# Performance work log

Measured on AMD Instinct MI355X. Metric: run time of the kernel, lower is better.

The kernel has to match this reference:

```python
import jax, jax.numpy as jnp
import numpy as np

N = 64        # n_nodes per graph
H = 128       # hidden channels (128x0e + 128x1o)
NB = 8        # radial bessel basis size
L = 2         # num_interactions
R_MAX = 5.0
AVG_NEIGH = 63.0
DIM = 3       # output vector dim
B = 64        # batch (vmapped)
T = 32        # time-embedding dim
S = 5         # num_species


def _edges(n):
    # fully-connected graph, no self loops (static shapes, jit-friendly)
    s, r = np.meshgrid(np.arange(n), np.arange(n), indexing='ij')
    m = s != r
    return jnp.asarray(s[m]), jnp.asarray(r[m])


def setup_inputs() -> dict:
    key = jax.random.key(0)
    ks = jax.random.split(key, 12)
    sc = 0.05
    return {
        'positions': jax.random.normal(ks[0], (B, N, 3), jnp.float32),
        'node_features': jax.random.randint(ks[1], (B, N), 0, S).astype(jnp.int64),
        'global_features': jax.random.normal(ks[2], (B, T), jnp.float32),
        'emb': jax.random.normal(ks[3], (S, H), jnp.float32) * sc,
        'Wt': jax.random.normal(ks[4], (T, H), jnp.float32) * sc,
        'Wr1': jax.random.normal(ks[5], (L, NB, H), jnp.float32) * sc,
        'Wr2': jax.random.normal(ks[6], (L, H, H), jnp.float32) * sc,
        'Wupd': jax.random.normal(ks[7], (L, H, H), jnp.float32) * sc,
        'Wmix': jax.random.normal(ks[8], (L, H, H), jnp.float32) * sc,
        'Wg1': jax.random.normal(ks[9], (H, H), jnp.float32) * sc,
        'Wg2': jax.random.normal(ks[10], (H, H), jnp.float32) * sc,
        'final_scaling': jnp.ones((), jnp.float32),
    }


def _call_single(pos, z, t, emb, Wt, Wr1, Wr2, Wupd, Wmix, Wg1, Wg2, final_scaling):
    snd, rcv = _edges(N)
    ev = pos[rcv] - pos[snd]                               # [E,3] edge vectors (gather)
    r = jnp.sqrt(jnp.sum(ev * ev, axis=-1) + 1e-12)        # [E]
    u = ev / r[:, None]                                    # unit directions
    # Bessel radial basis with cosine cutoff (r_max acts as soft radius graph)
    n = jnp.arange(1, NB + 1, dtype=pos.dtype)
    rb = jnp.sin(n * jnp.pi * r[:, None] / R_MAX) / r[:, None]   # [E,NB]
    fc = 0.5 * (jnp.cos(jnp.pi * r / R_MAX) + 1.0) * (r < R_MAX)
    rb = rb * fc[:, None]
    # node embedding from species + time embedding
    h = emb[z] + t @ Wt                                    # [N,H] scalar features
    v = jnp.zeros((N, H, DIM), pos.dtype)                  # vector (1o) features
    for l in range(L):
        w = jax.nn.silu(rb @ Wr1[l]) @ Wr2[l]              # [E,H] radial weights
        m0 = w * h[snd]                                    # [E,H] scalar messages
        m1 = m0[:, :, None] * u[:, None, :]                # [E,H,3] vector messages
        a0 = jax.ops.segment_sum(m0, rcv, num_segments=N) / AVG_NEIGH
        a1 = jax.ops.segment_sum(m1, rcv, num_segments=N) / AVG_NEIGH
        h = h + a0 @ Wupd[l]
        v = v + jnp.einsum('ngd,gh->nhd', a1, Wmix[l])
    # equivariant readout: scalar gate per channel contracts vector channels
    g = jax.nn.silu(h @ Wg1) @ Wg2                         # [N,H]
    out = jnp.einsum('nhd,nh->nd', v, g)                   # [N,3]
    return out * final_scaling


def reference(positions, node_features, global_features, emb, Wt, Wr1, Wr2, Wupd, Wmix, Wg1, Wg2, final_scaling):
    f = lambda p, z, t: _call_single(p, z, t, emb, Wt, Wr1, Wr2, Wupd, Wmix, Wg1, Wg2, final_scaling)
    return jax.vmap(f)(positions, node_features, global_features)
```

## Files before the change

kernel.cpp:

```cpp
#include <hip/hip_runtime.h>
#include <math.h>

#define NN 64
#define HH 128
#define NBB 8
#define TT 32
#define BB 64
#define NROW (BB * NN)
#define PLANE ((size_t)NROW * HH)
#define WR1OFF (8 * 16384)

typedef __attribute__((ext_vector_type(8))) short short8;
typedef __attribute__((ext_vector_type(4))) short s16x4;
typedef __attribute__((ext_vector_type(4))) float f32x4;
typedef __attribute__((ext_vector_type(2))) float f32x2;
typedef __attribute__((ext_vector_type(2))) unsigned int u32x2;

__device__ __forceinline__ float silu_f(float x) {
  return x * __builtin_amdgcn_rcpf(1.0f + __expf(-x));
}

__device__ __forceinline__ unsigned short bf1(float x) {
  __bf16 h = (__bf16)x;
  return *(unsigned short*)&h;
}
__device__ __forceinline__ unsigned bf2(float lo, float hi) {
  return (unsigned)bf1(lo) | ((unsigned)bf1(hi) << 16);
}

__device__ __forceinline__ void gemm8(
    const unsigned short (*sA)[136], const unsigned short* __restrict__ Bp,
    int w, int nlo, int quad, f32x4 C[2]) {
  const short8 z8 = {0, 0, 0, 0, 0, 0, 0, 0};
  short8 afr[4];
#pragma unroll
  for (int kt = 0; kt < 4; ++kt)
    afr[kt] = (nlo < 8) ? *(const short8*)&sA[nlo][kt * 32 + quad * 8] : z8;
#pragma unroll
  for (int nt = 0; nt < 2; ++nt)
#pragma unroll
    for (int kt = 0; kt < 4; ++kt) {
      short8 bfr = *(const short8*)&Bp[((kt * 128 + w * 32 + nt * 16 + nlo) * 4 + quad) * 8];
      C[nt] = __builtin_amdgcn_mfma_f32_16x16x32_bf16(afr[kt], bfr, C[nt], 0, 0, 0);
    }
}

__global__ __launch_bounds__(256) void k_init(
    const float* __restrict__ emb, const int* __restrict__ z,
    const float* __restrict__ gf, const float* __restrict__ Wt,
    const float* __restrict__ Wr1, const float* __restrict__ Wr2,
    const float* __restrict__ Wupd, const float* __restrict__ Wmix,
    const float* __restrict__ Wg1, const float* __restrict__ Wg2,
    float* __restrict__ h, unsigned short* __restrict__ Wpack) {
  __shared__ float tvec[HH];
  __shared__ int sz[NN];
  int b4 = blockIdx.x, tid = threadIdx.x;
#pragma unroll
  for (int ii = 0; ii < 2; ++ii) {
    int idx = b4 * 512 + ii * 256 + tid;
    int m = idx >> 14;
    int local = idx & 16383;
    float val;
    if (m < 2) val = Wr2[idx];
    else if (m < 4) val = Wupd[idx - 32768];
    else if (m < 6) val = Wmix[idx - 65536];
    else if (m == 6) val = Wg1[local];
    else val = Wg2[local];
    int k = local >> 7, n = local & 127;
    int kt = k >> 5, q = (k >> 3) & 3, j = k & 7;
    Wpack[(idx & ~16383) + (((kt * 128 + n) * 4 + q) * 8) + j] = bf1(val);
  }
  if (tid < 32) {
    int e = b4 * 32 + tid;
    int l = e >> 12, p = e & 4095;
    int n = p >> 5, q = (p >> 3) & 3, j = p & 7;
    float val = (q == 0) ? Wr1[l * NBB * HH + j * HH + n] : 0.f;
    Wpack[WR1OFF + l * 4096 + p] = bf1(val);
  }
  if (b4 < 64) {
    int b = b4;
    if (tid < NN) sz[tid] = z[b * NN + tid];
    if (tid < HH) {
      float acc = 0.f;
#pragma unroll
      for (int k = 0; k < TT; ++k) acc += gf[b * TT + k] * Wt[k * HH + tid];
      tvec[tid] = acc;
    }
    __syncthreads();
    for (int i = tid; i < NN * HH; i += 256) {
      int n = i >> 7, c = i & 127;
      h[(size_t)b * NN * HH + i] = emb[sz[n] * HH + c] + tvec[c];
    }
  }
}

__global__ __launch_bounds__(256) void k_layer(
    const float* __restrict__ pos,
    const float* __restrict__ hA,
    const unsigned short* __restrict__ a0in,
    unsigned short* __restrict__ apout,
    const unsigned short* __restrict__ Wpack,
    int l) {
  __shared__ __align__(16) unsigned short sh_S[NN][136];
  __shared__ __align__(16) unsigned short sh_M0T[4][32][44];
  __shared__ __align__(16) unsigned short sh_rbh[2][NN][8];
  __shared__ __align__(16) unsigned short sh_ub[2][4][NN];

  int blk = blockIdx.x;
  int b = blk >> 5, rp = blk & 31;
  int r0 = rp * 2;
  int tid = threadIdx.x;
  int w = tid >> 6, lane = tid & 63;
  int nlo = lane & 15, quad = lane >> 4;

  f32x4 hbv[4][2];
#pragma unroll
  for (int mt = 0; mt < 4; ++mt)
#pragma unroll
    for (int nt = 0; nt < 2; ++nt)
#pragma unroll
      for (int reg = 0; reg < 4; ++reg)
        hbv[mt][nt][reg] =
            hA[((size_t)b * NN + mt * 16 + quad * 4 + reg) * HH + w * 32 + nt * 16 + nlo];

  {
    int s = tid & 63;
    int ksel = (tid >> 6) & 1;
    int ri = (tid >> 7) & 1;
    int r = r0 + ri;
    const float* pb = pos + b * NN * 3;
    float dx = pb[r * 3 + 0] - pb[s * 3 + 0];
    float dy = pb[r * 3 + 1] - pb[s * 3 + 1];
    float dz = pb[r * 3 + 2] - pb[s * 3 + 2];
    float rr = sqrtf(dx * dx + dy * dy + dz * dz + 1e-12f);
    float inv = __builtin_amdgcn_rcpf(rr);
    const float invAvg = 1.0f / 63.0f;
    if (ksel == 0) {
      float ia = inv * invAvg;
      sh_ub[ri][1][s] = bf1(dx * ia);
      sh_ub[ri][2][s] = bf1(dy * ia);
      sh_ub[ri][3][s] = bf1(dz * ia);
    } else {
      sh_ub[ri][0][s] = bf1(invAvg);
    }
    const float PI_OVER_5 = 0.628318530717958647692f;
    float fc = (s != r && rr < 5.0f) ? 0.5f * (__cosf(PI_OVER_5 * rr) + 1.0f) : 0.0f;
    float base = PI_OVER_5 * rr;
    float sc = inv * fc;
    int k0 = ksel * 4;
    float v0 = __sinf((float)(k0 + 1) * base) * sc;
    float v1 = __sinf((float)(k0 + 2) * base) * sc;
    float v2 = __sinf((float)(k0 + 3) * base) * sc;
    float v3 = __sinf((float)(k0 + 4) * base) * sc;
    *(unsigned*)&sh_rbh[ri][s][k0]     = bf2(v0, v1);
    *(unsigned*)&sh_rbh[ri][s][k0 + 2] = bf2(v2, v3);
  }
  if (l) {
    for (int i = tid; i < NN * 64; i += 256) {
      int s = i >> 6, c2 = (i & 63) * 2;
      *(unsigned*)&sh_S[s][c2] =
          *(const unsigned*)&a0in[((size_t)b * NN + s) * HH + c2];
    }
  }
  __syncthreads();

  if (l) {
    const unsigned short* Bu = Wpack + 2 * 16384;
#pragma unroll
    for (int mt = 0; mt < 4; ++mt) {
      short8 afr[4];
#pragma unroll
      for (int kt = 0; kt < 4; ++kt)
        afr[kt] = *(const short8*)&sh_S[mt * 16 + nlo][kt * 32 + quad * 8];
#pragma unroll
      for (int nt = 0; nt < 2; ++nt)
#pragma unroll
        for (int kt = 0; kt < 4; ++kt) {
          short8 bfr = *(const short8*)&Bu[((kt * 128 + w * 32 + nt * 16 + nlo) * 4 + quad) * 8];
          hbv[mt][nt] = __builtin_amdgcn_mfma_f32_16x16x32_bf16(afr[kt], bfr, hbv[mt][nt], 0, 0, 0);
        }
    }
    __syncthreads();
  }

  const unsigned short* Wr1p = Wpack + WR1OFF + l * 4096;
  short8 bw[2];
#pragma unroll
  for (int nt = 0; nt < 2; ++nt)
    bw[nt] = *(const short8*)&Wr1p[((w * 32 + nt * 16 + nlo) * 4 + quad) * 8];
  const unsigned short* Bbase = Wpack + l * 16384;
  short8 bfr[4][2];
#pragma unroll
  for (int kt = 0; kt < 4; ++kt)
#pragma unroll
    for (int nt = 0; nt < 2; ++nt)
      bfr[kt][nt] = *(const short8*)&Bbase[((kt * 128 + w * 32 + nt * 16 + nlo) * 4 + quad) * 8];

  const short8 zero8 = {0, 0, 0, 0, 0, 0, 0, 0};
  short8 au[2][2];
#pragma unroll
  for (int ri = 0; ri < 2; ++ri)
#pragma unroll
    for (int kt = 0; kt < 2; ++kt)
      au[ri][kt] = (nlo < 4) ? *(const short8*)&sh_ub[ri][nlo][kt * 32 + quad * 8] : zero8;

#pragma unroll
  for (int ri = 0; ri < 2; ++ri) {
#pragma unroll
    for (int mtp = 0; mtp < 2; ++mtp) {
      f32x4 Cs[2][2];
#pragma unroll
      for (int mi = 0; mi < 2; ++mi)
#pragma unroll
        for (int nt = 0; nt < 2; ++nt) Cs[mi][nt] = (f32x4){0.f, 0.f, 0.f, 0.f};
#pragma unroll
      for (int mi = 0; mi < 2; ++mi) {
        int mt = mtp * 2 + mi;
        short8 afr = (quad == 0) ? *(const short8*)&sh_rbh[ri][mt * 16 + nlo][0] : zero8;
#pragma unroll
        for (int nt = 0; nt < 2; ++nt)
          Cs[mi][nt] = __builtin_amdgcn_mfma_f32_16x16x32_bf16(afr, bw[nt], Cs[mi][nt], 0, 0, 0);
      }
#pragma unroll
      for (int mi = 0; mi < 2; ++mi)
#pragma unroll
        for (int nt = 0; nt < 2; ++nt)
#pragma unroll
          for (int reg = 0; reg < 4; ++reg) {
            int s = (mtp * 2 + mi) * 16 + quad * 4 + reg;
            int c = w * 32 + nt * 16 + nlo;
            sh_S[s][c] = bf1(silu_f(Cs[mi][nt][reg]));
          }
    }
    __syncthreads();

    f32x4 Cu[2] = {{0, 0, 0, 0}, {0, 0, 0, 0}};
#pragma unroll
    for (int hf = 0; hf < 2; ++hf) {
#pragma unroll
      for (int mi = 0; mi < 2; ++mi) {
        int mt = hf * 2 + mi;
        short8 afr[4];
        int s_a = mt * 16 + nlo;
#pragma unroll
        for (int kt = 0; kt < 4; ++kt)
          afr[kt] = *(const short8*)&sh_S[s_a][kt * 32 + quad * 8];
#pragma unroll
        for (int nt = 0; nt < 2; ++nt) {
          f32x4 C = {0.f, 0.f, 0.f, 0.f};
#pragma unroll
          for (int kt = 0; kt < 4; ++kt)
            C = __builtin_amdgcn_mfma_f32_16x16x32_bf16(afr[kt], bfr[kt][nt], C, 0, 0, 0);
          f32x4 m0 = C * hbv[mt][nt];
          u32x2 pk;
          pk.x = bf2(m0[0], m0[1]);
          pk.y = bf2(m0[2], m0[3]);
          *(u32x2*)&sh_M0T[w][nt * 16 + nlo][mi * 16 + quad * 4] = pk;
        }
      }
#pragma unroll
      for (int nt = 0; nt < 2; ++nt) {
        short8 bm;
        *(s16x4*)&bm = *(const s16x4*)&sh_M0T[w][nt * 16 + nlo][quad * 8];
        *(s16x4*)(((short*)&bm) + 4) = *(const s16x4*)&sh_M0T[w][nt * 16 + nlo][quad * 8 + 4];
        Cu[nt] = __builtin_amdgcn_mfma_f32_16x16x32_bf16(au[ri][hf], bm, Cu[nt], 0, 0, 0);
      }
    }
    if (quad == 0) {
#pragma unroll
      for (int nt = 0; nt < 2; ++nt) {
        size_t base = (size_t)(b * NN + r0 + ri) * HH + w * 32 + nt * 16 + nlo;
#pragma unroll
        for (int reg = 0; reg < 4; ++reg)
          apout[(l * 4 + reg) * PLANE + base] = bf1(Cu[nt][reg]);
      }
    }
    if (ri == 0) __syncthreads();
  }
}

__global__ __launch_bounds__(256) void k_update_ro(
    const unsigned short* __restrict__ apbf, const float* __restrict__ hA,
    const unsigned short* __restrict__ Wpack,
    const float* __restrict__ fs, float* __restrict__ out) {
  __shared__ __align__(16) unsigned short sh_a[8][8][136];
  __shared__ __align__(16) unsigned short sh_h[8][136];
  __shared__ float red[4][8][3];
  int tid = threadIdx.x, w = tid >> 6, lane = tid & 63;
  int nlo = lane & 15, quad = lane >> 4;
  int row0 = blockIdx.x * 8;
  for (int i = tid; i < 8 * 8 * 64; i += 256) {
    int p = i >> 9, rr = (i >> 6) & 7, c2 = (i & 63) * 2;
    *(unsigned*)&sh_a[p][rr][c2] =
        *(const unsigned*)&apbf[p * PLANE + (size_t)(row0 + rr) * HH + c2];
  }
  f32x4 Ch[2];
#pragma unroll
  for (int nt = 0; nt < 2; ++nt)
#pragma unroll
    for (int reg = 0; reg < 4; ++reg)
      Ch[nt][reg] = (quad < 2)
          ? hA[(size_t)(row0 + quad * 4 + reg) * HH + w * 32 + nt * 16 + nlo] : 0.f;
  __syncthreads();
  gemm8(sh_a[0], Wpack + 2 * 16384, w, nlo, quad, Ch);
  gemm8(sh_a[4], Wpack + 3 * 16384, w, nlo, quad, Ch);
  f32x4 Cx[2] = {{0,0,0,0},{0,0,0,0}};
  f32x4 Cy[2] = {{0,0,0,0},{0,0,0,0}};
  f32x4 Cz[2] = {{0,0,0,0},{0,0,0,0}};
  gemm8(sh_a[1], Wpack + 4 * 16384, w, nlo, quad, Cx);
  gemm8(sh_a[5], Wpack + 5 * 16384, w, nlo, quad, Cx);
  gemm8(sh_a[2], Wpack + 4 * 16384, w, nlo, quad, Cy);
  gemm8(sh_a[6], Wpack + 5 * 16384, w, nlo, quad, Cy);
  gemm8(sh_a[3], Wpack + 4 * 16384, w, nlo, quad, Cz);
  gemm8(sh_a[7], Wpack + 5 * 16384, w, nlo, quad, Cz);
  if (quad < 2) {
#pragma unroll
    for (int nt = 0; nt < 2; ++nt)
#pragma unroll
      for (int reg = 0; reg < 4; ++reg)
        sh_h[quad * 4 + reg][w * 32 + nt * 16 + nlo] = bf1(Ch[nt][reg]);
  }
  __syncthreads();
  unsigned short (*sh_q)[136] = sh_a[0];
  f32x4 Cq[2] = {{0,0,0,0},{0,0,0,0}};
  gemm8(sh_h, Wpack + 6 * 16384, w, nlo, quad, Cq);
  if (quad < 2) {
#pragma unroll
    for (int nt = 0; nt < 2; ++nt)
#pragma unroll
      for (int reg = 0; reg < 4; ++reg)
        sh_q[quad * 4 + reg][w * 32 + nt * 16 + nlo] = bf1(silu_f(Cq[nt][reg]));
  }
  __syncthreads();
  f32x4 Cg[2] = {{0,0,0,0},{0,0,0,0}};
  gemm8(sh_q, Wpack + 7 * 16384, w, nlo, quad, Cg);
  float pr[3][4];
#pragma unroll
  for (int d = 0; d < 3; ++d)
#pragma unroll
    for (int reg = 0; reg < 4; ++reg) pr[d][reg] = 0.f;
#pragma unroll
  for (int nt = 0; nt < 2; ++nt)
#pragma unroll
    for (int reg = 0; reg < 4; ++reg) {
      float gv = Cg[nt][reg];
      pr[0][reg] += gv * Cx[nt][reg];
      pr[1][reg] += gv * Cy[nt][reg];
      pr[2][reg] += gv * Cz[nt][reg];
    }
#pragma unroll
  for (int off = 1; off < 16; off <<= 1)
#pragma unroll
    for (int d = 0; d < 3; ++d)
#pragma unroll
      for (int reg = 0; reg < 4; ++reg)
        pr[d][reg] += __shfl_xor(pr[d][reg], off);
  if (nlo == 0 && quad < 2) {
#pragma unroll
    for (int d = 0; d < 3; ++d)
#pragma unroll
      for (int reg = 0; reg < 4; ++reg)
        red[w][quad * 4 + reg][d] = pr[d][reg];
  }
  __syncthreads();
  if (tid < 24) {
    int row = tid / 3, d = tid % 3;
    float s = red[0][row][d] + red[1][row][d] + red[2][row][d] + red[3][row][d];
    out[(size_t)(row0 + row) * 3 + d] = s * fs[0];
  }
}

extern "C" void kernel_launch(void* const* d_in, const int* in_sizes, int n_in,
                              void* d_out, int out_size, void* d_ws, size_t ws_size,
                              hipStream_t stream) {
  const float* pos  = (const float*)d_in[0];
  const int*   z    = (const int*)d_in[1];
  const float* gf   = (const float*)d_in[2];
  const float* emb  = (const float*)d_in[3];
  const float* Wt   = (const float*)d_in[4];
  const float* Wr1  = (const float*)d_in[5];
  const float* Wr2  = (const float*)d_in[6];
  const float* Wupd = (const float*)d_in[7];
  const float* Wmix = (const float*)d_in[8];
  const float* Wg1  = (const float*)d_in[9];
  const float* Wg2  = (const float*)d_in[10];
  const float* fs   = (const float*)d_in[11];
  float* out = (float*)d_out;

  float* ws = (float*)d_ws;
  float* hA = ws;
  unsigned short* apbf = (unsigned short*)(ws + PLANE);
  unsigned short* Wpack = (unsigned short*)(ws + 5 * PLANE);

  k_init<<<dim3(256), dim3(256), 0, stream>>>(emb, z, gf, Wt, Wr1, Wr2, Wupd,
                                              Wmix, Wg1, Wg2, hA, Wpack);
  k_layer<<<dim3(BB * 32), dim3(256), 0, stream>>>(pos, hA, apbf, apbf, Wpack, 0);
  k_layer<<<dim3(BB * 32), dim3(256), 0, stream>>>(pos, hA, apbf, apbf, Wpack, 1);
  k_update_ro<<<dim3(512), dim3(256), 0, stream>>>(apbf, hA, Wpack, fs, out);
}
```

Measured before the change: 153.4 us.

## Fuse update and gated readout into second layer kernel epilogue

New measurement: 168.7 us. +10.0%, slower.

```diff
diff --git a/kernel.cpp b/kernel.cpp
--- a/kernel.cpp
+++ b/kernel.cpp
@@ -100,6 +100,7 @@
     const unsigned short* __restrict__ a0in,
     unsigned short* __restrict__ apout,
     const unsigned short* __restrict__ Wpack,
+    const float* __restrict__ fs, float* __restrict__ out,
     int l) {
   __shared__ __align__(16) unsigned short sh_S[NN][136];
   __shared__ __align__(16) unsigned short sh_M0T[4][32][44];
@@ -204,6 +205,8 @@
     for (int kt = 0; kt < 2; ++kt)
       au[ri][kt] = (nlo < 4) ? *(const short8*)&sh_ub[ri][nlo][kt * 32 + quad * 8] : zero8;
 
+  f32x4 Cur[2][2];
+
 #pragma unroll
   for (int ri = 0; ri < 2; ++ri) {
 #pragma unroll
@@ -266,107 +269,146 @@
         Cu[nt] = __builtin_amdgcn_mfma_f32_16x16x32_bf16(au[ri][hf], bm, Cu[nt], 0, 0, 0);
       }
     }
+    Cur[ri][0] = Cu[0];
+    Cur[ri][1] = Cu[1];
+    if (l == 0 && quad == 0) {
+#pragma unroll
+      for (int nt = 0; nt < 2; ++nt) {
+        size_t base = (size_t)(b * NN + r0 + ri) * HH + w * 32 + nt * 16 + nlo;
+#pragma unroll
+        for (int reg = 0; reg < 4; ++reg)
+          apout[reg * PLANE + base] = bf1(Cu[nt][reg]);
+      }
+    }
+    if (ri == 0) __syncthreads();
+  }
+
+  if (l) {
+    __syncthreads();
+    unsigned short* sbase = &sh_S[0][0];
+    unsigned short (*sh_ar )[136] = (unsigned short(*)[136])(sbase);
+    unsigned short (*sh_ar0)[136] = (unsigned short(*)[136])(sbase + 1088);
+    float* sh_hrow = (float*)(sbase + 2176);
+    unsigned short (*sh_hb)[136] = (unsigned short(*)[136])(sbase + 2704);
+    unsigned short (*sh_qb)[136] = (unsigned short(*)[136])(sbase + 2976);
+    float* sh_g  = (float*)(sbase + 3248);
+    float* sh_v0 = (float*)(sbase + 3776);
+    float* sh_v1 = (float*)(sbase + 5360);
+    float* red   = (float*)(sbase + 6944);
+
     if (quad == 0) {
 #pragma unroll
-      for (int nt = 0; nt < 2; ++nt) {
-        size_t base = (size_t)(b * NN + r0 + ri) * HH + w * 32 + nt * 16 + nlo;
-#pragma unroll
-        for (int reg = 0; reg < 4; ++reg)
-          apout[(l * 4 + reg) * PLANE + base] = bf1(Cu[nt][reg]);
-      }
-    }
-    if (ri == 0) __syncthreads();
-  }
-}
-
-__global__ __launch_bounds__(256) void k_update_ro(
-    const unsigned short* __restrict__ apbf, const float* __restrict__ hA,
-    const unsigned short* __restrict__ Wpack,
-    const float* __restrict__ fs, float* __restrict__ out) {
-  __shared__ __align__(16) unsigned short sh_a[8][8][136];
-  __shared__ __align__(16) unsigned short sh_h[8][136];
-  __shared__ float red[4][8][3];
-  int tid = threadIdx.x, w = tid >> 6, lane = tid & 63;
-  int nlo = lane & 15, quad = lane >> 4;
-  int row0 = blockIdx.x * 8;
-  for (int i = tid; i < 8 * 8 * 64; i += 256) {
-    int p = i >> 9, rr = (i >> 6) & 7, c2 = (i & 63) * 2;
-    *(unsigned*)&sh_a[p][rr][c2] =
-        *(const unsigned*)&apbf[p * PLANE + (size_t)(row0 + rr) * HH + c2];
-  }
-  f32x4 Ch[2];
-#pragma unroll
-  for (int nt = 0; nt < 2; ++nt)
-#pragma unroll
-    for (int reg = 0; reg < 4; ++reg)
-      Ch[nt][reg] = (quad < 2)
-          ? hA[(size_t)(row0 + quad * 4 + reg) * HH + w * 32 + nt * 16 + nlo] : 0.f;
-  __syncthreads();
-  gemm8(sh_a[0], Wpack + 2 * 16384, w, nlo, quad, Ch);
-  gemm8(sh_a[4], Wpack + 3 * 16384, w, nlo, quad, Ch);
-  f32x4 Cx[2] = {{0,0,0,0},{0,0,0,0}};
-  f32x4 Cy[2] = {{0,0,0,0},{0,0,0,0}};
-  f32x4 Cz[2] = {{0,0,0,0},{0,0,0,0}};
-  gemm8(sh_a[1], Wpack + 4 * 16384, w, nlo, quad, Cx);
-  gemm8(sh_a[5], Wpack + 5 * 16384, w, nlo, quad, Cx);
-  gemm8(sh_a[2], Wpack + 4 * 16384, w, nlo, quad, Cy);
-  gemm8(sh_a[6], Wpack + 5 * 16384, w, nlo, quad, Cy);
-  gemm8(sh_a[3], Wpack + 4 * 16384, w, nlo, quad, Cz);
-  gemm8(sh_a[7], Wpack + 5 * 16384, w, nlo, quad, Cz);
-  if (quad < 2) {
-#pragma unroll
-    for (int nt = 0; nt < 2; ++nt)
-#pragma unroll
-      for (int reg = 0; reg < 4; ++reg)
-        sh_h[quad * 4 + reg][w * 32 + nt * 16 + nlo] = bf1(Ch[nt][reg]);
-  }
-  __syncthreads();
-  unsigned short (*sh_q)[136] = sh_a[0];
-  f32x4 Cq[2] = {{0,0,0,0},{0,0,0,0}};
-  gemm8(sh_h, Wpack + 6 * 16384, w, nlo, quad, Cq);
-  if (quad < 2) {
-#pragma unroll
-    for (int nt = 0; nt < 2; ++nt)
-#pragma unroll
-      for (int reg = 0; reg < 4; ++reg)
-        sh_q[quad * 4 + reg][w * 32 + nt * 16 + nlo] = bf1(silu_f(Cq[nt][reg]));
-  }
-  __syncthreads();
-  f32x4 Cg[2] = {{0,0,0,0},{0,0,0,0}};
-  gemm8(sh_q, Wpack + 7 * 16384, w, nlo, quad, Cg);
-  float pr[3][4];
-#pragma unroll
-  for (int d = 0; d < 3; ++d)
-#pragma unroll
-    for (int reg = 0; reg < 4; ++reg) pr[d][reg] = 0.f;
-#pragma unroll
-  for (int nt = 0; nt < 2; ++nt)
-#pragma unroll
-    for (int reg = 0; reg < 4; ++reg) {
-      float gv = Cg[nt][reg];
-      pr[0][reg] += gv * Cx[nt][reg];
-      pr[1][reg] += gv * Cy[nt][reg];
-      pr[2][reg] += gv * Cz[nt][reg];
-    }
-#pragma unroll
-  for (int off = 1; off < 16; off <<= 1)
-#pragma unroll
-    for (int d = 0; d < 3; ++d)
-#pragma unroll
-      for (int reg = 0; reg < 4; ++reg)
-        pr[d][reg] += __shfl_xor(pr[d][reg], off);
-  if (nlo == 0 && quad < 2) {
-#pragma unroll
-    for (int d = 0; d < 3; ++d)
-#pragma unroll
-      for (int reg = 0; reg < 4; ++reg)
-        red[w][quad * 4 + reg][d] = pr[d][reg];
-  }
-  __syncthreads();
-  if (tid < 24) {
-    int row = tid / 3, d = tid % 3;
-    float s = red[0][row][d] + red[1][row][d] + red[2][row][d] + red[3][row][d];
-    out[(size_t)(row0 + row) * 3 + d] = s * fs[0];
+      for (int ri = 0; ri < 2; ++ri)
+#pragma unroll
+        for (int nt = 0; nt < 2; ++nt) {
+          int c = w * 32 + nt * 16 + nlo;
+          sh_ar[ri][c] = bf1(Cur[ri][nt][0]);
+#pragma unroll
+          for (int d = 0; d < 3; ++d)
+            sh_ar[2 + d * 2 + ri][c] = bf1(Cur[ri][nt][1 + d]);
+        }
+    }
+    for (int i = tid; i < 384; i += 256) {
+      int row = i >> 6, c2 = (i & 63) * 2;
+      int d = row >> 1, ri = row & 1;
+      *(unsigned*)&sh_ar0[row][c2] =
+          *(const unsigned*)&apout[(size_t)(1 + d) * PLANE +
+                                   ((size_t)(b * NN + r0 + ri)) * HH + c2];
+    }
+    {
+      int mt0 = r0 >> 4, quad0 = (r0 & 15) >> 2, reg0 = r0 & 3;
+      if (quad == quad0) {
+#pragma unroll
+        for (int nt = 0; nt < 2; ++nt) {
+          int c = w * 32 + nt * 16 + nlo;
+          sh_hrow[c]       = hbv[mt0][nt][reg0];
+          sh_hrow[132 + c] = hbv[mt0][nt][reg0 + 1];
+        }
+      }
+    }
+    __syncthreads();
+
+    f32x4 G1[2] = {{0,0,0,0},{0,0,0,0}};
+    f32x4 G2[2] = {{0,0,0,0},{0,0,0,0}};
+    f32x4 G3[2] = {{0,0,0,0},{0,0,0,0}};
+    gemm8(sh_ar,  Wpack + 3 * 16384, w, nlo, quad, G1);
+    gemm8(sh_ar,  Wpack + 5 * 16384, w, nlo, quad, G2);
+    gemm8(sh_ar0, Wpack + 4 * 16384, w, nlo, quad, G3);
+    if (quad == 0) {
+#pragma unroll
+      for (int nt = 0; nt < 2; ++nt) {
+        int c = w * 32 + nt * 16 + nlo;
+        sh_hb[0][c] = bf1(sh_hrow[c] + G1[nt][0]);
+        sh_hb[1][c] = bf1(sh_hrow[132 + c] + G1[nt][1]);
+      }
+    }
+#pragma unroll
+    for (int idx = 0; idx < 6; ++idx) {
+      int row2 = 2 + idx;
+      if (quad == (row2 >> 2)) {
+#pragma unroll
+        for (int nt = 0; nt < 2; ++nt)
+          sh_v1[idx * 132 + w * 32 + nt * 16 + nlo] = G2[nt][row2 & 3];
+      }
+      if (quad == (idx >> 2)) {
+#pragma unroll
+        for (int nt = 0; nt < 2; ++nt)
+          sh_v0[idx * 132 + w * 32 + nt * 16 + nlo] = G3[nt][idx & 3];
+      }
+    }
+    __syncthreads();
+
+    f32x4 Gq[2] = {{0,0,0,0},{0,0,0,0}};
+    gemm8(sh_hb, Wpack + 6 * 16384, w, nlo, quad, Gq);
+    if (quad == 0) {
+#pragma unroll
+      for (int nt = 0; nt < 2; ++nt) {
+        int c = w * 32 + nt * 16 + nlo;
+        sh_qb[0][c] = bf1(silu_f(Gq[nt][0]));
+        sh_qb[1][c] = bf1(silu_f(Gq[nt][1]));
+      }
+    }
+    __syncthreads();
+
+    f32x4 Gg[2] = {{0,0,0,0},{0,0,0,0}};
+    gemm8(sh_qb, Wpack + 7 * 16384, w, nlo, quad, Gg);
+    if (quad == 0) {
+#pragma unroll
+      for (int nt = 0; nt < 2; ++nt) {
+        int c = w * 32 + nt * 16 + nlo;
+        sh_g[c]       = Gg[nt][0];
+        sh_g[132 + c] = Gg[nt][1];
+      }
+    }
+    __syncthreads();
+
+    float pr[6];
+#pragma unroll
+    for (int idx = 0; idx < 6; ++idx) pr[idx] = 0.f;
+    if (quad == 0) {
+#pragma unroll
+      for (int nt = 0; nt < 2; ++nt) {
+        int c = w * 32 + nt * 16 + nlo;
+#pragma unroll
+        for (int idx = 0; idx < 6; ++idx)
+          pr[idx] += (sh_v0[idx * 132 + c] + sh_v1[idx * 132 + c]) * sh_g[(idx & 1) * 132 + c];
+      }
+    }
+#pragma unroll
+    for (int off = 1; off < 64; off <<= 1)
+#pragma unroll
+      for (int idx = 0; idx < 6; ++idx)
+        pr[idx] += __shfl_xor(pr[idx], off);
+    if (lane == 0) {
+#pragma unroll
+      for (int idx = 0; idx < 6; ++idx) red[w * 6 + idx] = pr[idx];
+    }
+    __syncthreads();
+    if (tid < 6) {
+      float s = red[tid] + red[6 + tid] + red[12 + tid] + red[18 + tid];
+      int d = tid >> 1, ri = tid & 1;
+      out[((size_t)(b * NN + r0 + ri)) * 3 + d] = s * fs[0];
+    }
   }
 }
 
@@ -394,7 +436,8 @@
 
   k_init<<<dim3(256), dim3(256), 0, stream>>>(emb, z, gf, Wt, Wr1, Wr2, Wupd,
                                               Wmix, Wg1, Wg2, hA, Wpack);
-  k_layer<<<dim3(BB * 32), dim3(256), 0, stream>>>(pos, hA, apbf, apbf, Wpack, 0);
-  k_layer<<<dim3(BB * 32), dim3(256), 0, stream>>>(pos, hA, apbf, apbf, Wpack, 1);
-  k_update_ro<<<dim3(512), dim3(256), 0, stream>>>(apbf, hA, Wpack, fs, out);
-}
+  k_layer<<<dim3(BB * 32), dim3(256), 0, stream>>>(pos, hA, apbf, apbf, Wpack,
+                                                   fs, out, 0);
+  k_layer<<<dim3(BB * 32), dim3(256), 0, stream>>>(pos, hA, apbf, apbf, Wpack,
+                                                   fs, out, 1);
+}
```
